# Performance work log

Measured on AMD Instinct MI355X. Metric: run time of the kernel, lower is better.

The kernel has to match this reference:

```python
import jax, jax.numpy as jnp
import numpy as np

WINDOW_SIZE = 64  # matches init_kwargs


def _local_allowed_mask(L, window_size):
    # Original torch code: for query i, keys in slice [max(i-w//2,0) : min(i+w//2, L)) are allowed.
    half = window_size // 2
    i = jnp.arange(L)[:, None]
    j = jnp.arange(L)[None, :]
    return (j >= i - half) & (j < i + half)  # [L, L] bool, True = attend


def setup_inputs() -> dict:
    key = jax.random.key(0)
    kq, kk, kv = jax.random.split(key, 3)
    B, L, H, E, D = 4, 2048, 16, 64, 64
    queries = jax.random.normal(kq, (B, L, H, E), dtype=jnp.float32)
    keys = jax.random.normal(kk, (B, L, H, E), dtype=jnp.float32)
    values = jax.random.normal(kv, (B, L, H, D), dtype=jnp.float32)
    attn_mask = jnp.zeros((1,), dtype=bool)  # unused by the module
    return {"queries": queries, "keys": keys, "values": values, "attn_mask": attn_mask}


def reference(queries, keys, values, attn_mask):
    B, L, H, E = queries.shape
    scale = 1.0 / np.sqrt(E).astype(np.float32)
    allowed = _local_allowed_mask(L, WINDOW_SIZE)  # [L, L]
    # Dense scores, as in the original module (einsum 'blhe,bshe->bhls')
    scores = jnp.einsum('blhe,bshe->bhls', queries, keys)
    neg_inf = jnp.asarray(-jnp.inf, dtype=scores.dtype)
    scores = jnp.where(allowed[None, None, :, :], scores, neg_inf)
    A = jax.nn.softmax(scale * scores, axis=-1)  # [B, H, L, S]
    V = jnp.einsum('bhls,bshd->blhd', A, values)  # [B, L, H, D]
    return V
```

## Files before the change

kernel.cpp:

```cpp
#include <hip/hip_runtime.h>


#define B_ 4
#define L_ 2048
#define H_ 16
#define E_ 64
#define D_ 64

#define QS_STRIDE 72
#define KS_STRIDE 72
#define VT_STRIDE 152
#define P_STRIDE 104

typedef __attribute__((ext_vector_type(8))) short short8;
typedef __attribute__((ext_vector_type(4))) float f32x4;

__device__ __forceinline__ unsigned int f2bf(float x) {
  unsigned int b = __float_as_uint(x);
  b += 0x7fffu + ((b >> 16) & 1u);
  return b >> 16;
}
__device__ __forceinline__ unsigned int pack2(float a, float b) {
  return f2bf(a) | (f2bf(b) << 16);
}

__global__ __launch_bounds__(256, 2)
void local_attn_mfma(const float* __restrict__ qg,
                     const float* __restrict__ kg,
                     const float* __restrict__ vg,
                     float* __restrict__ og) {
  __shared__ __align__(16) unsigned short Qs[64 * QS_STRIDE];
  __shared__ __align__(16) unsigned short Ks[128 * KS_STRIDE];
  __shared__ __align__(16) unsigned short Vt[64 * VT_STRIDE];
  __shared__ __align__(16) unsigned short Pl[4 * 16 * P_STRIDE];

  const int t = threadIdx.x;
  const int q0 = blockIdx.x * 64;
  const int h = blockIdx.y;
  const int b = blockIdx.z;
  const int kstart = q0 - 32;

  #pragma unroll
  for (int it = 0; it < 8; ++it) {
    int cid = t + it * 256;
    int row = cid >> 4, ch = cid & 15;
    int key = kstart + row;
    float4 f = make_float4(0.f, 0.f, 0.f, 0.f);
    if (key >= 0 && key < L_)
      f = *(const float4*)(kg + ((size_t)(b * L_ + key) * H_ + h) * E_ + ch * 4);
    uint2 p = make_uint2(pack2(f.x, f.y), pack2(f.z, f.w));
    *(uint2*)&Ks[row * KS_STRIDE + ch * 4] = p;
  }
  #pragma unroll
  for (int it = 0; it < 4; ++it) {
    int cid = t + it * 256;
    int row = cid >> 4, ch = cid & 15;
    float4 f = *(const float4*)(qg + ((size_t)(b * L_ + q0 + row) * H_ + h) * E_ + ch * 4);
    uint2 p = make_uint2(pack2(f.x, f.y), pack2(f.z, f.w));
    *(uint2*)&Qs[row * QS_STRIDE + ch * 4] = p;
  }
  {
    int kp = t >> 2;
    int dq = t & 3;
    int k0 = kstart + 2 * kp, k1 = k0 + 1;
    float4 a[4], c[4];
    #pragma unroll
    for (int i = 0; i < 4; ++i) {
      a[i] = make_float4(0.f, 0.f, 0.f, 0.f);
      c[i] = make_float4(0.f, 0.f, 0.f, 0.f);
    }
    if (k0 >= 0 && k0 < L_) {
      const float* p = vg + ((size_t)(b * L_ + k0) * H_ + h) * D_ + dq * 16;
      #pragma unroll
      for (int i = 0; i < 4; ++i) a[i] = *(const float4*)(p + i * 4);
    }
    if (k1 >= 0 && k1 < L_) {
      const float* p = vg + ((size_t)(b * L_ + k1) * H_ + h) * D_ + dq * 16;
      #pragma unroll
      for (int i = 0; i < 4; ++i) c[i] = *(const float4*)(p + i * 4);
    }
    #pragma unroll
    for (int i = 0; i < 4; ++i) {
      float av[4] = {a[i].x, a[i].y, a[i].z, a[i].w};
      float cv[4] = {c[i].x, c[i].y, c[i].z, c[i].w};
      #pragma unroll
      for (int j = 0; j < 4; ++j) {
        int d = dq * 16 + i * 4 + j;
        *(unsigned int*)&Vt[d * VT_STRIDE + 2 * kp] = pack2(av[j], cv[j]);
      }
    }
    int zr = t >> 2, zc = 128 + (t & 3) * 4;
    *(uint2*)&Vt[zr * VT_STRIDE + zc] = make_uint2(0u, 0u);
  }
  __syncthreads();

  const int wave = t >> 6;
  const int lane = t & 63;
  const int col16 = lane & 15;
  const int quad = lane >> 4;

  const short8 qa0 = *(const short8*)&Qs[(wave * 16 + col16) * QS_STRIDE + quad * 8];
  const short8 qa1 = *(const short8*)&Qs[(wave * 16 + col16) * QS_STRIDE + quad * 8 + 32];

  f32x4 acc[5];
  #pragma unroll
  for (int tt = 0; tt < 5; ++tt) {
    int krow = wave * 16 + tt * 16 + col16;
    short8 b0 = *(const short8*)&Ks[krow * KS_STRIDE + quad * 8];
    short8 b1 = *(const short8*)&Ks[krow * KS_STRIDE + quad * 8 + 32];
    f32x4 c = {0.f, 0.f, 0.f, 0.f};
    c = __builtin_amdgcn_mfma_f32_16x16x32_bf16(qa0, b0, c, 0, 0, 0);
    c = __builtin_amdgcn_mfma_f32_16x16x32_bf16(qa1, b1, c, 0, 0, 0);
    acc[tt] = c;
  }

  #pragma unroll
  for (int r = 0; r < 4; ++r) {
    const int row_loc = quad * 4 + r;
    float x[5];
    #pragma unroll
    for (int tt = 0; tt < 5; ++tt) {
      int c_loc = tt * 16 + col16;
      int gkey = kstart + wave * 16 + c_loc;
      bool ok = (c_loc >= row_loc) && (c_loc < row_loc + 64) && (gkey >= 0) && (gkey < L_);
      x[tt] = ok ? acc[tt][r] * 0.125f : -1e30f;
    }
    float m = fmaxf(fmaxf(fmaxf(x[0], x[1]), fmaxf(x[2], x[3])), x[4]);
    m = fmaxf(m, __shfl_xor(m, 1));
    m = fmaxf(m, __shfl_xor(m, 2));
    m = fmaxf(m, __shfl_xor(m, 4));
    m = fmaxf(m, __shfl_xor(m, 8));
    float s = 0.f;
    #pragma unroll
    for (int tt = 0; tt < 5; ++tt) { x[tt] = __expf(x[tt] - m); s += x[tt]; }
    s += __shfl_xor(s, 1);
    s += __shfl_xor(s, 2);
    s += __shfl_xor(s, 4);
    s += __shfl_xor(s, 8);
    float inv = 1.0f / s;
    #pragma unroll
    for (int tt = 0; tt < 5; ++tt) acc[tt][r] = x[tt] * inv;
  }

  unsigned short* Pw = &Pl[wave * 16 * P_STRIDE];
  *(uint2*)&Pw[col16 * P_STRIDE + 80 + quad * 4] = make_uint2(0u, 0u);
  #pragma unroll
  for (int tt = 0; tt < 5; ++tt)
    #pragma unroll
    for (int r = 0; r < 4; ++r)
      Pw[(quad * 4 + r) * P_STRIDE + tt * 16 + col16] = (unsigned short)f2bf(acc[tt][r]);

  f32x4 oacc[4];
  #pragma unroll
  for (int nt = 0; nt < 4; ++nt) oacc[nt] = (f32x4){0.f, 0.f, 0.f, 0.f};
  #pragma unroll
  for (int ks = 0; ks < 3; ++ks) {
    short8 pa = *(const short8*)&Pw[col16 * P_STRIDE + ks * 32 + quad * 8];
    #pragma unroll
    for (int nt = 0; nt < 4; ++nt) {
      short8 vb = *(const short8*)&Vt[(nt * 16 + col16) * VT_STRIDE + wave * 16 + ks * 32 + quad * 8];
      oacc[nt] = __builtin_amdgcn_mfma_f32_16x16x32_bf16(pa, vb, oacc[nt], 0, 0, 0);
    }
  }

  #pragma unroll
  for (int r = 0; r < 4; ++r) {
    int q = q0 + wave * 16 + quad * 4 + r;
    float* orow = og + ((size_t)(b * L_ + q) * H_ + h) * D_;
    #pragma unroll
    for (int nt = 0; nt < 4; ++nt)
      orow[nt * 16 + col16] = oacc[nt][r];
  }
}

extern "C" void kernel_launch(void* const* d_in, const int* in_sizes, int n_in,
                              void* d_out, int out_size, void* d_ws, size_t ws_size,
                              hipStream_t stream) {
  const float* q = (const float*)d_in[0];
  const float* k = (const float*)d_in[1];
  const float* v = (const float*)d_in[2];
  float* o = (float*)d_out;
  dim3 grid(L_ / 64, H_, B_);
  local_attn_mfma<<<grid, dim3(256), 0, stream>>>(q, k, v, o);
}
```

Before: 151.1 us.

## Load Q and K fragments directly from global into registers, drop LDS staging

Q and K tiles are no longer staged through shared memory. Each lane loads its MFMA operand fragments straight from global memory and converts them to bf16 in registers. The V transpose is rewritten so each thread packs four keys per store, and the occupancy hint is raised from 2 to 4 blocks per CU now that LDS use is smaller. In exchange, K rows are loaded redundantly across waves (each wave reads 80 keys with overlap), and the tighter launch bound adds register pressure because 10 short8 K fragments are held live.

```diff
diff --git a/kernel.cpp b/kernel.cpp
--- a/kernel.cpp
+++ b/kernel.cpp
@@ -6,9 +6,6 @@
 #define H_ 16
 #define E_ 64
 #define D_ 64
-
-#define QS_STRIDE 72
-#define KS_STRIDE 72
 #define VT_STRIDE 152
 #define P_STRIDE 104
 
@@ -23,14 +20,17 @@
 __device__ __forceinline__ unsigned int pack2(float a, float b) {
   return f2bf(a) | (f2bf(b) << 16);
 }
+__device__ __forceinline__ short8 pack8(const float4& a, const float4& b) {
+  union { short8 s; uint4 u; } r;
+  r.u = make_uint4(pack2(a.x, a.y), pack2(a.z, a.w), pack2(b.x, b.y), pack2(b.z, b.w));
+  return r.s;
+}
 
-__global__ __launch_bounds__(256, 2)
+__global__ __launch_bounds__(256, 4)
 void local_attn_mfma(const float* __restrict__ qg,
                      const float* __restrict__ kg,
                      const float* __restrict__ vg,
                      float* __restrict__ og) {
-  __shared__ __align__(16) unsigned short Qs[64 * QS_STRIDE];
-  __shared__ __align__(16) unsigned short Ks[128 * KS_STRIDE];
   __shared__ __align__(16) unsigned short Vt[64 * VT_STRIDE];
   __shared__ __align__(16) unsigned short Pl[4 * 16 * P_STRIDE];
 
@@ -39,78 +39,71 @@
   const int h = blockIdx.y;
   const int b = blockIdx.z;
   const int kstart = q0 - 32;
-
-  #pragma unroll
-  for (int it = 0; it < 8; ++it) {
-    int cid = t + it * 256;
-    int row = cid >> 4, ch = cid & 15;
-    int key = kstart + row;
-    float4 f = make_float4(0.f, 0.f, 0.f, 0.f);
-    if (key >= 0 && key < L_)
-      f = *(const float4*)(kg + ((size_t)(b * L_ + key) * H_ + h) * E_ + ch * 4);
-    uint2 p = make_uint2(pack2(f.x, f.y), pack2(f.z, f.w));
-    *(uint2*)&Ks[row * KS_STRIDE + ch * 4] = p;
-  }
-  #pragma unroll
-  for (int it = 0; it < 4; ++it) {
-    int cid = t + it * 256;
-    int row = cid >> 4, ch = cid & 15;
-    float4 f = *(const float4*)(qg + ((size_t)(b * L_ + q0 + row) * H_ + h) * E_ + ch * 4);
-    uint2 p = make_uint2(pack2(f.x, f.y), pack2(f.z, f.w));
-    *(uint2*)&Qs[row * QS_STRIDE + ch * 4] = p;
-  }
-  {
-    int kp = t >> 2;
-    int dq = t & 3;
-    int k0 = kstart + 2 * kp, k1 = k0 + 1;
-    float4 a[4], c[4];
-    #pragma unroll
-    for (int i = 0; i < 4; ++i) {
-      a[i] = make_float4(0.f, 0.f, 0.f, 0.f);
-      c[i] = make_float4(0.f, 0.f, 0.f, 0.f);
-    }
-    if (k0 >= 0 && k0 < L_) {
-      const float* p = vg + ((size_t)(b * L_ + k0) * H_ + h) * D_ + dq * 16;
-      #pragma unroll
-      for (int i = 0; i < 4; ++i) a[i] = *(const float4*)(p + i * 4);
-    }
-    if (k1 >= 0 && k1 < L_) {
-      const float* p = vg + ((size_t)(b * L_ + k1) * H_ + h) * D_ + dq * 16;
-      #pragma unroll
-      for (int i = 0; i < 4; ++i) c[i] = *(const float4*)(p + i * 4);
-    }
-    #pragma unroll
-    for (int i = 0; i < 4; ++i) {
-      float av[4] = {a[i].x, a[i].y, a[i].z, a[i].w};
-      float cv[4] = {c[i].x, c[i].y, c[i].z, c[i].w};
-      #pragma unroll
-      for (int j = 0; j < 4; ++j) {
-        int d = dq * 16 + i * 4 + j;
-        *(unsigned int*)&Vt[d * VT_STRIDE + 2 * kp] = pack2(av[j], cv[j]);
-      }
-    }
-    int zr = t >> 2, zc = 128 + (t & 3) * 4;
-    *(uint2*)&Vt[zr * VT_STRIDE + zc] = make_uint2(0u, 0u);
-  }
-  __syncthreads();
-
   const int wave = t >> 6;
   const int lane = t & 63;
   const int col16 = lane & 15;
   const int quad = lane >> 4;
 
-  const short8 qa0 = *(const short8*)&Qs[(wave * 16 + col16) * QS_STRIDE + quad * 8];
-  const short8 qa1 = *(const short8*)&Qs[(wave * 16 + col16) * QS_STRIDE + quad * 8 + 32];
+  {
+    const int kq = t & 31;
+    const int dg = t >> 5;
+    float va[4][8];
+    #pragma unroll
+    for (int u = 0; u < 4; ++u) {
+      int key = kstart + 4 * kq + u;
+      float4 fa = make_float4(0.f, 0.f, 0.f, 0.f);
+      float4 fb = make_float4(0.f, 0.f, 0.f, 0.f);
+      if (key >= 0 && key < L_) {
+        const float* p = vg + ((size_t)(b * L_ + key) * H_ + h) * D_ + dg * 8;
+        fa = *(const float4*)p;
+        fb = *(const float4*)(p + 4);
+      }
+      va[u][0] = fa.x; va[u][1] = fa.y; va[u][2] = fa.z; va[u][3] = fa.w;
+      va[u][4] = fb.x; va[u][5] = fb.y; va[u][6] = fb.z; va[u][7] = fb.w;
+    }
+    #pragma unroll
+    for (int i = 0; i < 8; ++i) {
+      uint2 w = make_uint2(pack2(va[0][i], va[1][i]), pack2(va[2][i], va[3][i]));
+      *(uint2*)&Vt[(dg * 8 + i) * VT_STRIDE + 4 * kq] = w;
+    }
+    *(uint2*)&Vt[(t >> 2) * VT_STRIDE + 128 + (t & 3) * 4] = make_uint2(0u, 0u);
+  }
+
+  short8 qa0, qa1;
+  {
+    const float* p = qg + ((size_t)(b * L_ + q0 + wave * 16 + col16) * H_ + h) * E_ + quad * 8;
+    float4 a0 = *(const float4*)p;
+    float4 a1 = *(const float4*)(p + 4);
+    float4 a2 = *(const float4*)(p + 32);
+    float4 a3 = *(const float4*)(p + 36);
+    qa0 = pack8(a0, a1);
+    qa1 = pack8(a2, a3);
+  }
+
+  short8 kb0[5], kb1[5];
+  #pragma unroll
+  for (int tt = 0; tt < 5; ++tt) {
+    int key = kstart + wave * 16 + tt * 16 + col16;
+    float4 a0 = make_float4(0.f, 0.f, 0.f, 0.f);
+    float4 a1 = a0, a2 = a0, a3 = a0;
+    if (key >= 0 && key < L_) {
+      const float* p = kg + ((size_t)(b * L_ + key) * H_ + h) * E_ + quad * 8;
+      a0 = *(const float4*)p;
+      a1 = *(const float4*)(p + 4);
+      a2 = *(const float4*)(p + 32);
+      a3 = *(const float4*)(p + 36);
+    }
+    kb0[tt] = pack8(a0, a1);
+    kb1[tt] = pack8(a2, a3);
+  }
+  __syncthreads();
 
   f32x4 acc[5];
   #pragma unroll
   for (int tt = 0; tt < 5; ++tt) {
-    int krow = wave * 16 + tt * 16 + col16;
-    short8 b0 = *(const short8*)&Ks[krow * KS_STRIDE + quad * 8];
-    short8 b1 = *(const short8*)&Ks[krow * KS_STRIDE + quad * 8 + 32];
     f32x4 c = {0.f, 0.f, 0.f, 0.f};
-    c = __builtin_amdgcn_mfma_f32_16x16x32_bf16(qa0, b0, c, 0, 0, 0);
-    c = __builtin_amdgcn_mfma_f32_16x16x32_bf16(qa1, b1, c, 0, 0, 0);
+    c = __builtin_amdgcn_mfma_f32_16x16x32_bf16(qa0, kb0[tt], c, 0, 0, 0);
+    c = __builtin_amdgcn_mfma_f32_16x16x32_bf16(qa1, kb1[tt], c, 0, 0, 0);
     acc[tt] = c;
   }
 
```

Result: no change. 148.3 us (-1.8%).
